# Kernel tuning notes

Measured on AMD Instinct MI355X. Metric: run time of the kernel, lower is better.

The kernel has to match this reference:

```python
import jax, jax.numpy as jnp
import numpy as np

# Constants from module-level env defaults
CONST_VAL = 10.0                       # VLLM_SOFTMAX_CONST_VAL
EPS = 1.1754943508222875e-38           # torch.finfo(torch.bfloat16).tiny
SCALE = 0.08838834764831845            # 1/sqrt(head_size=128)

B, QH, KVH, D = 32, 32, 8, 128         # batch, q heads, kv heads, head dim
NUM_CACHE_BLOCKS, BLOCK_SIZE = 600, 128
BLOCKS_PER_SEQ = 16                    # context 2048 / block_size 128
NB = B * BLOCKS_PER_SEQ                # 512 active blocks


def setup_inputs() -> dict:
    key = jax.random.key(0)
    ks = jax.random.split(key, 6)
    query = jax.random.normal(ks[0], (B, QH, D), dtype=jnp.float32)
    key_cache = jax.random.normal(ks[1], (NUM_CACHE_BLOCKS, BLOCK_SIZE, KVH, D), dtype=jnp.float32)
    value_cache = jax.random.normal(ks[2], (NUM_CACHE_BLOCKS, BLOCK_SIZE, KVH, D), dtype=jnp.float32)
    # each active block points at a distinct physical cache block
    block_list = jax.random.permutation(ks[3], NUM_CACHE_BLOCKS)[:NB].astype(jnp.int32)
    # block i belongs to sequence i // BLOCKS_PER_SEQ -> one-hot [NB, B]
    block_to_batch = jnp.arange(NB) // BLOCKS_PER_SEQ
    block_mapping = jax.nn.one_hot(block_to_batch, B, dtype=jnp.float32)
    # ALiBi-like per-position bias within each block (non-positive)
    block_bias = -5.0 * jax.random.uniform(ks[4], (NB, BLOCK_SIZE), dtype=jnp.float32)
    return {
        'query': query,
        'key_cache': key_cache,
        'value_cache': value_cache,
        'block_mapping': block_mapping,
        'block_bias': block_bias,
        'block_list': block_list,
    }


def reference(query, key_cache, value_cache, block_mapping, block_bias, block_list):
    """flat_pa decode path with the pa() const-norm softmax normalization (GQA)."""
    b, qh, d = query.shape
    kvh = key_cache.shape[2]
    g = qh // kvh                                   # queries per kv head
    nb, bs = block_bias.shape
    # batch2block(scale * query): [NB,B] @ [B, QH, D] -> [NB, QH, D]
    q = jnp.einsum('nb,bhd->nhd', block_mapping, SCALE * query)
    q = q.reshape(nb, kvh, g, 1, d)                 # [NB, KVH, G, 1, D]
    k = key_cache[block_list]                       # [NB, BS, KVH, D]
    v = value_cache[block_list]                     # [NB, BS, KVH, D]
    # attn = q @ k^T + block_bias : [NB, KVH, G, 1, BS]
    attn = jnp.einsum('nkgqd,nskd->nkgqs', q, k)
    attn = attn + block_bias[:, None, None, None, :]
    # const-norm exp (no running max; subtract fixed const)
    attn = jnp.exp(attn - CONST_VAL)
    block_sum = attn.sum(axis=-1, keepdims=True)    # [NB, KVH, G, 1, 1]
    # block2batch then batch2block: per-sequence sum broadcast back to blocks
    group_sums = jnp.einsum('nb,nkgqo->bkgqo', block_mapping, block_sum)
    group_sums = jnp.einsum('nb,bkgqo->nkgqo', block_mapping, group_sums) + EPS
    group_sums = jnp.maximum(block_sum, group_sums)
    attn = attn / group_sums
    out = jnp.einsum('nkgqs,nskd->nkgqd', attn, v)  # [NB, KVH, G, 1, D]
    # block2batch: accumulate per-block partial outputs into per-sequence output
    out = jnp.einsum('nb,nkgqd->bkgqd', block_mapping, out)
    return out.reshape(b, qh, d)                    # squeeze q-dim, flatten heads
```

## Files before the change

### kernel.cpp

```cpp
#include <hip/hip_runtime.h>

#define NBATCH 32
#define QH 32
#define KVH 8
#define G 4
#define DH 128
#define BS 128
#define NB 512
#define CONST_VAL 10.0f
#define EPS_T 1.1754943508222875e-38f
#define SCALE_F 0.08838834764831845f


__global__ void pa_zero_S(float* S) {
    int i = blockIdx.x * 256 + threadIdx.x;
    if (i < NBATCH * KVH * G) S[i] = 0.f;
}

__global__ __launch_bounds__(256) void pa_pass1(
    const float* __restrict__ query,
    const float* __restrict__ key_cache,
    const float* __restrict__ value_cache,
    const float* __restrict__ mapping,
    const float* __restrict__ bias,
    const int*   __restrict__ block_list,
    float* __restrict__ partial,
    float* __restrict__ bsum,
    float* __restrict__ S)
{
    const int n  = blockIdx.x;
    const int kh = blockIdx.y;
    const int t  = threadIdx.x;

    __shared__ float sW[NBATCH];
    __shared__ float sQ[G][DH];
    __shared__ float sKV[64][129];
    __shared__ float sE[G][BS];
    __shared__ float sBs[G];

    if (t < NBATCH) sW[t] = mapping[n * NBATCH + t];
    __syncthreads();

    {
        int i0 = t, i1 = t + 256;
        int g0 = i0 >> 7, d0 = i0 & 127;
        int g1 = i1 >> 7, d1 = i1 & 127;
        float qa = 0.f, qb = 0.f;
        for (int b = 0; b < NBATCH; ++b) {
            float w = sW[b];
            if (w != 0.f) {
                const float* qrow = query + ((size_t)b * QH + (size_t)kh * G) * DH;
                qa += w * qrow[g0 * DH + d0];
                qb += w * qrow[g1 * DH + d1];
            }
        }
        sQ[g0][d0] = qa * SCALE_F;
        sQ[g1][d1] = qb * SCALE_F;
    }

    const int p = block_list[n];
    const float* kbase = key_cache   + (size_t)p * BS * KVH * DH + (size_t)kh * DH;
    const float* vbase = value_cache + (size_t)p * BS * KVH * DH + (size_t)kh * DH;
    const int row_stride = KVH * DH;

    const int s_l = t & 63;
    const int g_s = t >> 6;
    for (int ph = 0; ph < 2; ++ph) {
        __syncthreads();
        for (int i = 0; i < 8; ++i) {
            int j = i * 256 + t;
            int row = j >> 5;
            int c4  = j & 31;
            float4 kv = *(const float4*)(kbase + (size_t)(ph * 64 + row) * row_stride + c4 * 4);
            float* dst = &sKV[row][c4 * 4];
            dst[0] = kv.x; dst[1] = kv.y; dst[2] = kv.z; dst[3] = kv.w;
        }
        __syncthreads();
        float acc = 0.f;
        #pragma unroll 8
        for (int d = 0; d < DH; ++d) acc += sKV[s_l][d] * sQ[g_s][d];
        int s = ph * 64 + s_l;
        sE[g_s][s] = __expf(acc + bias[(size_t)n * BS + s] - CONST_VAL);
    }
    __syncthreads();

    {
        int wave = t >> 6, lane = t & 63;
        float v = sE[wave][lane] + sE[wave][lane + 64];
        for (int off = 32; off > 0; off >>= 1) v += __shfl_down(v, off);
        if (lane == 0) sBs[wave] = v;
    }
    __syncthreads();
    if (t < G) {
        float bsv = sBs[t];
        bsum[((size_t)n * KVH + kh) * G + t] = bsv;
        for (int b = 0; b < NBATCH; ++b) {
            float w = sW[b];
            if (w != 0.f) atomicAdd(&S[(b * KVH + kh) * G + t], w * bsv);
        }
    }

    const int d_v = t & 127;
    const int gg  = t >> 7;
    float o0 = 0.f, o1 = 0.f;
    for (int ph = 0; ph < 2; ++ph) {
        __syncthreads();
        for (int i = 0; i < 8; ++i) {
            int j = i * 256 + t;
            int row = j >> 5;
            int c4  = j & 31;
            float4 vv = *(const float4*)(vbase + (size_t)(ph * 64 + row) * row_stride + c4 * 4);
            float* dst = &sKV[row][c4 * 4];
            dst[0] = vv.x; dst[1] = vv.y; dst[2] = vv.z; dst[3] = vv.w;
        }
        __syncthreads();
        int g0 = gg * 2, g1 = gg * 2 + 1;
        #pragma unroll 8
        for (int sl = 0; sl < 64; ++sl) {
            float v = sKV[sl][d_v];
            int s = ph * 64 + sl;
            o0 += sE[g0][s] * v;
            o1 += sE[g1][s] * v;
        }
    }
    size_t pb = (((size_t)n * KVH + kh) * G) * DH;
    partial[pb + (size_t)(gg * 2)     * DH + d_v] = o0;
    partial[pb + (size_t)(gg * 2 + 1) * DH + d_v] = o1;
}

__global__ __launch_bounds__(256) void pa_den(
    const float* __restrict__ mapping,
    const float* __restrict__ bsum,
    const float* __restrict__ S,
    float* __restrict__ den)
{
    int i = blockIdx.x * 256 + threadIdx.x;
    if (i >= NB * KVH * G) return;
    int g  = i & (G - 1);
    int kh = (i / G) & (KVH - 1);
    int n  = i / (G * KVH);
    float gs = 0.f;
    for (int b = 0; b < NBATCH; ++b)
        gs += mapping[n * NBATCH + b] * S[(b * KVH + kh) * G + g];
    gs += EPS_T;
    den[i] = fmaxf(bsum[i], gs);
}

__global__ __launch_bounds__(256) void pa_pass2(
    const float* __restrict__ mapping,
    const float* __restrict__ partial,
    const float* __restrict__ den,
    float* __restrict__ out)
{
    int b  = blockIdx.x;
    int kh = blockIdx.y;
    int t  = threadIdx.x;
    int g  = t >> 7;
    int d  = t & 127;

    __shared__ float sWc[NB];
    for (int i = t; i < NB; i += 256) sWc[i] = mapping[i * NBATCH + b];
    __syncthreads();

    float a0 = 0.f, a1 = 0.f;
    for (int n = 0; n < NB; ++n) {
        float w = sWc[n];
        if (w == 0.f) continue;
        int di = (n * KVH + kh) * G;
        size_t pb = (size_t)di * DH;
        a0 += w * partial[pb + (size_t)g * DH + d] / den[di + g];
        a1 += w * partial[pb + (size_t)(g + 2) * DH + d] / den[di + g + 2];
    }
    size_t ob = ((size_t)b * QH + (size_t)kh * G) * DH;
    out[ob + (size_t)g * DH + d]       = a0;
    out[ob + (size_t)(g + 2) * DH + d] = a1;
}

extern "C" void kernel_launch(void* const* d_in, const int* in_sizes, int n_in,
                              void* d_out, int out_size, void* d_ws, size_t ws_size,
                              hipStream_t stream) {
    const float* query       = (const float*)d_in[0];
    const float* key_cache   = (const float*)d_in[1];
    const float* value_cache = (const float*)d_in[2];
    const float* mapping     = (const float*)d_in[3];
    const float* bias        = (const float*)d_in[4];
    const int*   block_list  = (const int*)d_in[5];
    float* out = (float*)d_out;

    float* partial = (float*)d_ws;
    float* bsum    = partial + (size_t)NB * KVH * G * DH;
    float* S       = bsum + (size_t)NB * KVH * G;
    float* den     = S + (size_t)NBATCH * KVH * G;

    pa_zero_S<<<4, 256, 0, stream>>>(S);
    pa_pass1<<<dim3(NB, KVH), 256, 0, stream>>>(
        query, key_cache, value_cache, mapping, bias, block_list, partial, bsum, S);
    pa_den<<<(NB * KVH * G + 255) / 256, 256, 0, stream>>>(mapping, bsum, S, den);
    pa_pass2<<<dim3(NBATCH, KVH), 256, 0, stream>>>(mapping, partial, den, out);
}
```

Baseline: 630.9 us.

## Rewrite pass1 as single-wave register-resident fused QK/softmax/PV with prefetch

Replaces the 256-thread shared-memory pass1 with a 64-lane single-wave kernel. Each 16-lane group handles one token row and keeps K/V float4 fragments in registers, reducing dot products through cross-lane shuffles and fusing exp and the PV accumulation in one streaming pass. K and V for the next row are prefetched (double buffering) so no LDS staging or barriers are needed, and K/V are read only once per element. The cost is higher register pressure and extra shuffle reductions, plus fewer threads per block, which may reduce latency hiding.

```diff
diff --git a/kernel.cpp b/kernel.cpp
--- a/kernel.cpp
+++ b/kernel.cpp
@@ -12,12 +12,67 @@
 #define SCALE_F 0.08838834764831845f
 
 
+__device__ __forceinline__ float4 ld4(const float* __restrict__ p) {
+    return *(const float4* __restrict__)p;
+}
+__device__ __forceinline__ void fma4(float4& o, float a, float4 v) {
+    o.x = fmaf(a, v.x, o.x);
+    o.y = fmaf(a, v.y, o.y);
+    o.z = fmaf(a, v.z, o.z);
+    o.w = fmaf(a, v.w, o.w);
+}
+__device__ __forceinline__ float dot8(float4 a0, float4 a1, float4 b0, float4 b1) {
+    float r = a0.x * b0.x;
+    r = fmaf(a0.y, b0.y, r);
+    r = fmaf(a0.z, b0.z, r);
+    r = fmaf(a0.w, b0.w, r);
+    r = fmaf(a1.x, b1.x, r);
+    r = fmaf(a1.y, b1.y, r);
+    r = fmaf(a1.z, b1.z, r);
+    r = fmaf(a1.w, b1.w, r);
+    return r;
+}
+__device__ __forceinline__ void redcross4(float4& v) {
+    v.x += __shfl_xor(v.x, 16); v.y += __shfl_xor(v.y, 16);
+    v.z += __shfl_xor(v.z, 16); v.w += __shfl_xor(v.w, 16);
+    v.x += __shfl_xor(v.x, 32); v.y += __shfl_xor(v.y, 32);
+    v.z += __shfl_xor(v.z, 32); v.w += __shfl_xor(v.w, 32);
+}
+
 __global__ void pa_zero_S(float* S) {
     int i = blockIdx.x * 256 + threadIdx.x;
     if (i < NBATCH * KVH * G) S[i] = 0.f;
 }
 
-__global__ __launch_bounds__(256) void pa_pass1(
+__device__ __forceinline__ void pa_step(
+    int step, int grp, float b_lo, float b_hi,
+    float4 k0, float4 k1, float4 v0, float4 v1,
+    const float4 (&qlo)[G], const float4 (&qhi)[G],
+    float4 (&oLo)[G], float4 (&oHi)[G], float (&es)[G])
+{
+    float pr[G];
+#pragma unroll
+    for (int g = 0; g < G; ++g)
+        pr[g] = dot8(qlo[g], qhi[g], k0, k1);
+#pragma unroll
+    for (int g = 0; g < G; ++g) {
+        pr[g] += __shfl_xor(pr[g], 1);
+        pr[g] += __shfl_xor(pr[g], 2);
+        pr[g] += __shfl_xor(pr[g], 4);
+        pr[g] += __shfl_xor(pr[g], 8);
+    }
+    const int s = step * 4 + grp;
+    const float bb = __shfl(step < 16 ? b_lo : b_hi, s & 63);
+#pragma unroll
+    for (int g = 0; g < G; ++g) {
+        float e = __expf(pr[g] + bb - CONST_VAL);
+        es[g] += e;
+        fma4(oLo[g], e, v0);
+        fma4(oHi[g], e, v1);
+    }
+}
+
+__global__ __launch_bounds__(64) void pa_pass1(
     const float* __restrict__ query,
     const float* __restrict__ key_cache,
     const float* __restrict__ value_cache,
@@ -28,104 +83,98 @@
     float* __restrict__ bsum,
     float* __restrict__ S)
 {
-    const int n  = blockIdx.x;
-    const int kh = blockIdx.y;
-    const int t  = threadIdx.x;
-
-    __shared__ float sW[NBATCH];
-    __shared__ float sQ[G][DH];
-    __shared__ float sKV[64][129];
-    __shared__ float sE[G][BS];
-    __shared__ float sBs[G];
-
-    if (t < NBATCH) sW[t] = mapping[n * NBATCH + t];
-    __syncthreads();
-
-    {
-        int i0 = t, i1 = t + 256;
-        int g0 = i0 >> 7, d0 = i0 & 127;
-        int g1 = i1 >> 7, d1 = i1 & 127;
-        float qa = 0.f, qb = 0.f;
-        for (int b = 0; b < NBATCH; ++b) {
-            float w = sW[b];
-            if (w != 0.f) {
-                const float* qrow = query + ((size_t)b * QH + (size_t)kh * G) * DH;
-                qa += w * qrow[g0 * DH + d0];
-                qb += w * qrow[g1 * DH + d1];
-            }
+    const int n    = blockIdx.x;
+    const int kh   = blockIdx.y;
+    const int lane = threadIdx.x;
+    const int grp  = lane >> 4;
+    const int c    = lane & 15;
+
+    float w = 0.f;
+    if (lane < NBATCH) w = mapping[n * NBATCH + lane];
+    const unsigned long long mball = __ballot(w != 0.f);
+
+    float4 qlo[G], qhi[G], oLo[G], oHi[G];
+    float  es[G];
+#pragma unroll
+    for (int g = 0; g < G; ++g) {
+        qlo[g] = make_float4(0.f, 0.f, 0.f, 0.f);
+        qhi[g] = make_float4(0.f, 0.f, 0.f, 0.f);
+        oLo[g] = make_float4(0.f, 0.f, 0.f, 0.f);
+        oHi[g] = make_float4(0.f, 0.f, 0.f, 0.f);
+        es[g]  = 0.f;
+    }
+
+    unsigned long long mm = mball;
+    while (mm) {
+        const int b = __ffsll(mm) - 1;
+        mm &= mm - 1;
+        const float wb = __shfl(w, b) * SCALE_F;
+        const float* qr = query + ((size_t)b * QH + (size_t)kh * G) * DH + 4 * c;
+#pragma unroll
+        for (int g = 0; g < G; ++g) {
+            fma4(qlo[g], wb, ld4(qr + g * DH));
+            fma4(qhi[g], wb, ld4(qr + g * DH + 64));
         }
-        sQ[g0][d0] = qa * SCALE_F;
-        sQ[g1][d1] = qb * SCALE_F;
-    }
+    }
+
+    const float b_lo = bias[(size_t)n * BS + lane];
+    const float b_hi = bias[(size_t)n * BS + 64 + lane];
 
     const int p = block_list[n];
-    const float* kbase = key_cache   + (size_t)p * BS * KVH * DH + (size_t)kh * DH;
-    const float* vbase = value_cache + (size_t)p * BS * KVH * DH + (size_t)kh * DH;
-    const int row_stride = KVH * DH;
-
-    const int s_l = t & 63;
-    const int g_s = t >> 6;
-    for (int ph = 0; ph < 2; ++ph) {
-        __syncthreads();
-        for (int i = 0; i < 8; ++i) {
-            int j = i * 256 + t;
-            int row = j >> 5;
-            int c4  = j & 31;
-            float4 kv = *(const float4*)(kbase + (size_t)(ph * 64 + row) * row_stride + c4 * 4);
-            float* dst = &sKV[row][c4 * 4];
-            dst[0] = kv.x; dst[1] = kv.y; dst[2] = kv.z; dst[3] = kv.w;
+    const size_t blk = (size_t)p * BS * KVH * DH + (size_t)kh * DH
+                     + (size_t)grp * (KVH * DH) + 4 * c;
+    const float* kb = key_cache   + blk;
+    const float* vb = value_cache + blk;
+    const int SSTRIDE = 4 * KVH * DH;
+
+    float4 kA0 = ld4(kb),      kA1 = ld4(kb + 64);
+    float4 vA0 = ld4(vb),      vA1 = ld4(vb + 64);
+
+    for (int it = 0; it < 16; ++it) {
+        const float* kpB = kb + (size_t)(2 * it + 1) * SSTRIDE;
+        const float* vpB = vb + (size_t)(2 * it + 1) * SSTRIDE;
+        float4 kB0 = ld4(kpB), kB1 = ld4(kpB + 64);
+        float4 vB0 = ld4(vpB), vB1 = ld4(vpB + 64);
+
+        pa_step(2 * it, grp, b_lo, b_hi, kA0, kA1, vA0, vA1,
+                qlo, qhi, oLo, oHi, es);
+
+        const int sA = (it < 15) ? (2 * it + 2) : 0;
+        const float* kpA = kb + (size_t)sA * SSTRIDE;
+        const float* vpA = vb + (size_t)sA * SSTRIDE;
+        kA0 = ld4(kpA); kA1 = ld4(kpA + 64);
+        vA0 = ld4(vpA); vA1 = ld4(vpA + 64);
+
+        pa_step(2 * it + 1, grp, b_lo, b_hi, kB0, kB1, vB0, vB1,
+                qlo, qhi, oLo, oHi, es);
+    }
+
+#pragma unroll
+    for (int g = 0; g < G; ++g) {
+        es[g] += __shfl_xor(es[g], 16);
+        es[g] += __shfl_xor(es[g], 32);
+        redcross4(oLo[g]);
+        redcross4(oHi[g]);
+    }
+
+    const size_t base = ((size_t)n * KVH + kh) * G;
+    if (lane == 0)
+        *(float4*)(bsum + base) = make_float4(es[0], es[1], es[2], es[3]);
+
+    if (w != 0.f) {
+#pragma unroll
+        for (int g = 0; g < G; ++g)
+            atomicAdd(&S[(lane * KVH + kh) * G + g], w * es[g]);
+    }
+
+    if (lane < 16) {
+        const size_t pb = base * DH;
+#pragma unroll
+        for (int g = 0; g < G; ++g) {
+            *(float4*)(partial + pb + (size_t)g * DH + 4 * c)      = oLo[g];
+            *(float4*)(partial + pb + (size_t)g * DH + 64 + 4 * c) = oHi[g];
         }
-        __syncthreads();
-        float acc = 0.f;
-        #pragma unroll 8
-        for (int d = 0; d < DH; ++d) acc += sKV[s_l][d] * sQ[g_s][d];
-        int s = ph * 64 + s_l;
-        sE[g_s][s] = __expf(acc + bias[(size_t)n * BS + s] - CONST_VAL);
-    }
-    __syncthreads();
-
-    {
-        int wave = t >> 6, lane = t & 63;
-        float v = sE[wave][lane] + sE[wave][lane + 64];
-        for (int off = 32; off > 0; off >>= 1) v += __shfl_down(v, off);
-        if (lane == 0) sBs[wave] = v;
-    }
-    __syncthreads();
-    if (t < G) {
-        float bsv = sBs[t];
-        bsum[((size_t)n * KVH + kh) * G + t] = bsv;
-        for (int b = 0; b < NBATCH; ++b) {
-            float w = sW[b];
-            if (w != 0.f) atomicAdd(&S[(b * KVH + kh) * G + t], w * bsv);
-        }
-    }
-
-    const int d_v = t & 127;
-    const int gg  = t >> 7;
-    float o0 = 0.f, o1 = 0.f;
-    for (int ph = 0; ph < 2; ++ph) {
-        __syncthreads();
-        for (int i = 0; i < 8; ++i) {
-            int j = i * 256 + t;
-            int row = j >> 5;
-            int c4  = j & 31;
-            float4 vv = *(const float4*)(vbase + (size_t)(ph * 64 + row) * row_stride + c4 * 4);
-            float* dst = &sKV[row][c4 * 4];
-            dst[0] = vv.x; dst[1] = vv.y; dst[2] = vv.z; dst[3] = vv.w;
-        }
-        __syncthreads();
-        int g0 = gg * 2, g1 = gg * 2 + 1;
-        #pragma unroll 8
-        for (int sl = 0; sl < 64; ++sl) {
-            float v = sKV[sl][d_v];
-            int s = ph * 64 + sl;
-            o0 += sE[g0][s] * v;
-            o1 += sE[g1][s] * v;
-        }
-    }
-    size_t pb = (((size_t)n * KVH + kh) * G) * DH;
-    partial[pb + (size_t)(gg * 2)     * DH + d_v] = o0;
-    partial[pb + (size_t)(gg * 2 + 1) * DH + d_v] = o1;
+    }
 }
 
 __global__ __launch_bounds__(256) void pa_den(
@@ -193,7 +242,7 @@
     float* den     = S + (size_t)NBATCH * KVH * G;
 
     pa_zero_S<<<4, 256, 0, stream>>>(S);
-    pa_pass1<<<dim3(NB, KVH), 256, 0, stream>>>(
+    pa_pass1<<<dim3(NB, KVH), 64, 0, stream>>>(
         query, key_cache, value_cache, mapping, bias, block_list, partial, bsum, S);
     pa_den<<<(NB * KVH * G + 255) / 256, 256, 0, stream>>>(mapping, bsum, S, den);
     pa_pass2<<<dim3(NBATCH, KVH), 256, 0, stream>>>(mapping, partial, den, out);
```

New measurement: 625.6 us. About the same (-0.8%).
